# Kernel optimization log

Measured on AMD Instinct MI355X. Metric: run time of the kernel, lower is better.

The kernel has to match this reference:

```python
import jax, jax.numpy as jnp
import numpy as np

EPS = 1e-06


def setup_inputs() -> dict:
    key = jax.random.key(0)
    k1, k2 = jax.random.split(key)
    x = jax.random.normal(k1, (256, 4096), dtype=jnp.float32)
    # learned parameter, init matches torch.randn(...) * 0.1
    shapelets = jax.random.normal(k2, (8, 16, 128), dtype=jnp.float32) * 0.1
    return {"x": x, "shapelets": shapelets}


def reference(x, shapelets):
    B, T = x.shape
    C, Kc, L = shapelets.shape
    nwin = T - L + 1  # stride-1 unfold

    # sliding windows: [B, nwin, L] (same materialization as torch unfold)
    idx = jnp.arange(nwin)[:, None] + jnp.arange(L)[None, :]
    x_win = x[:, idx]

    # z-normalize each window (population std, unbiased=False)
    mu_x = jnp.mean(x_win, axis=2, keepdims=True)
    var_x = jnp.mean((x_win - mu_x) ** 2, axis=2, keepdims=True)
    std_x = jnp.sqrt(var_x) + EPS
    x_norm = (x_win - mu_x) / std_x

    # z-normalize shapelets per class/shapelet
    mu_s = jnp.mean(shapelets, axis=2, keepdims=True)
    var_s = jnp.mean((shapelets - mu_s) ** 2, axis=2, keepdims=True)
    std_s = jnp.sqrt(var_s) + EPS
    s_norm = (shapelets - mu_s) / std_s

    # normalized cross-correlation: [B, nwin, C, Kc]
    corr = jnp.einsum('btl,ckl->btck', x_norm, s_norm) / L

    # max over window positions, concat classes -> [B, C*Kc]
    max_vals = jnp.max(corr, axis=1)  # [B, C, Kc]
    return max_vals.reshape(B, C * Kc)
```

## Files before the change

kernel.cpp:

```cpp
#include <hip/hip_runtime.h>
#include <hip/hip_bf16.h>

typedef __attribute__((ext_vector_type(8))) short short8;
typedef __attribute__((ext_vector_type(4))) float float4v;

#define T_LEN 4096
#define L_LEN 128
#define NWIN  3969
#define CK    128

__device__ __forceinline__ unsigned short f2bf(float f) {
    unsigned u = __float_as_uint(f);
    u += 0x7fffu + ((u >> 16) & 1u);
    return (unsigned short)(u >> 16);
}

__global__ void prep_sh(const float* __restrict__ sh,
                        unsigned short* __restrict__ wsB) {
    const int ck = blockIdx.x;
    const int l  = threadIdx.x;
    __shared__ float rs[2], rq[2];
    const int lane = l & 63, wv = l >> 6;

    float v = sh[ck * L_LEN + l];
    float s = v, q = v * v;
    #pragma unroll
    for (int off = 32; off >= 1; off >>= 1) {
        s += __shfl_xor(s, off);
        q += __shfl_xor(q, off);
    }
    if (lane == 0) { rs[wv] = s; rq[wv] = q; }
    __syncthreads();
    float sm = rs[0] + rs[1], sq = rq[0] + rq[1];
    float mu  = sm * (1.f / L_LEN);
    float var = fmaxf(sq * (1.f / L_LEN) - mu * mu, 0.f);
    float inv = 1.f / (sqrtf(var) + 1e-6f);
    unsigned short b = f2bf((v - mu) * inv);
    const int nt = ck >> 4, n = ck & 15;
    const int kt = l >> 5, qd = (l >> 3) & 3, jj = l & 7;
    wsB[((((nt * 4 + kt) * 64) + qd * 16 + n) << 3) + jj] = b;
}

__global__ __launch_bounds__(512, 2)
void conv_row(const float* __restrict__ x,
              const unsigned short* __restrict__ wsB,
              float* __restrict__ out) {
    __shared__ alignas(16) unsigned short xb[8][T_LEN];
    __shared__ float sty[T_LEN];
    __shared__ float PSs[513], PQs[513];
    __shared__ float grpS[8], grpQ[8];
    __shared__ float wmax[8][CK];

    const int tid  = threadIdx.x;
    const int lane = tid & 63;
    const int wv   = tid >> 6;
    const int row  = blockIdx.x;
    const float4* xr4 = (const float4*)(x + row * T_LEN);

    short8 Bf[8][4];
    {
        const short8* Bp = (const short8*)wsB;
        #pragma unroll
        for (int nt = 0; nt < 8; ++nt)
            #pragma unroll
            for (int kt = 0; kt < 4; ++kt)
                Bf[nt][kt] = Bp[(nt * 4 + kt) * 64 + lane];
    }

    float v[16];
    {
        float4 a0 = xr4[2 * tid];
        float4 a1 = xr4[2 * tid + 1];
        float4 a2 = make_float4(0.f, 0.f, 0.f, 0.f), a3 = a2;
        if (tid < 511) { a2 = xr4[2 * tid + 2]; a3 = xr4[2 * tid + 3]; }
        v[0]=a0.x; v[1]=a0.y; v[2]=a0.z;  v[3]=a0.w;
        v[4]=a1.x; v[5]=a1.y; v[6]=a1.z;  v[7]=a1.w;
        v[8]=a2.x; v[9]=a2.y; v[10]=a2.z; v[11]=a2.w;
        v[12]=a3.x; v[13]=a3.y; v[14]=a3.z; v[15]=a3.w;
    }
    unsigned short bb[16];
    #pragma unroll
    for (int i = 0; i < 16; ++i) bb[i] = f2bf(v[i]);
    #pragma unroll
    for (int c = 0; c < 8; ++c) {
        short8 w8;
        #pragma unroll
        for (int j = 0; j < 8; ++j) w8[j] = (short)bb[c + j];
        *(short8*)&xb[c][8 * tid] = w8;
    }

    float s = 0.f, q = 0.f;
    #pragma unroll
    for (int i = 0; i < 8; ++i) { s += v[i]; q += v[i] * v[i]; }
    float is = s, iq = q;
    #pragma unroll
    for (int off = 1; off < 64; off <<= 1) {
        float ts = __shfl_up(is, off);
        float tq = __shfl_up(iq, off);
        if (lane >= off) { is += ts; iq += tq; }
    }
    if (lane == 63) { grpS[wv] = is; grpQ[wv] = iq; }
    __syncthreads();
    float os = 0.f, oq = 0.f;
    #pragma unroll
    for (int w = 0; w < 7; ++w) if (w < wv) { os += grpS[w]; oq += grpQ[w]; }
    PSs[tid] = os + is - s;
    PQs[tid] = oq + iq - q;
    if (tid == 511) { PSs[512] = os + is; PQs[512] = oq + iq; }
    __syncthreads();

    if (tid < 497) {
        float S = PSs[tid + 16] - PSs[tid];
        float Q = PQs[tid + 16] - PQs[tid];
        float4 b0 = make_float4(0.f, 0.f, 0.f, 0.f), b1 = b0;
        if (tid <= 495) { b0 = xr4[2 * tid + 32]; b1 = xr4[2 * tid + 33]; }
        float xn[8] = {b0.x, b0.y, b0.z, b0.w, b1.x, b1.y, b1.z, b1.w};
        #pragma unroll
        for (int e = 0; e < 8; ++e) {
            int w = 8 * tid + e;
            if (w < NWIN) {
                float mu  = S * (1.f / L_LEN);
                float var = fmaxf(Q * (1.f / L_LEN) - mu * mu, 0.f);
                float sd  = sqrtf(var) + 1e-6f;
                sty[w] = 1.f / (sd * (float)L_LEN);
                S += xn[e] - v[e];
                Q += xn[e] * xn[e] - v[e] * v[e];
            }
        }
    }
    __syncthreads();

    const int abase = (lane & 15) + (lane >> 4);
    const int q4    = (lane >> 4) * 4;
    float vmax[8];
    #pragma unroll
    for (int nt = 0; nt < 8; ++nt) vmax[nt] = -1e30f;

    #pragma unroll 1
    for (int ci = 0; ci < 32; ++ci) {
        const int T0 = (ci < 31) ? ci * 128 : (NWIN - 128);
        const int e0 = T0 + wv;
        const int c  = e0 & 7;
        const int b8 = e0 >> 3;

        float4v acc[8];
        #pragma unroll
        for (int nt = 0; nt < 8; ++nt) acc[nt] = float4v{0.f, 0.f, 0.f, 0.f};

        #pragma unroll
        for (int kt = 0; kt < 4; ++kt) {
            const short8 af = *(const short8*)&xb[c][8 * (b8 + abase + 4 * kt)];
            #pragma unroll
            for (int nt = 0; nt < 8; ++nt)
                acc[nt] = __builtin_amdgcn_mfma_f32_16x16x32_bf16(
                    af, Bf[nt][kt], acc[nt], 0, 0, 0);
        }

        #pragma unroll
        for (int r = 0; r < 4; ++r) {
            const float sr = sty[e0 + 8 * (q4 + r)];
            #pragma unroll
            for (int nt = 0; nt < 8; ++nt)
                vmax[nt] = fmaxf(vmax[nt], acc[nt][r] * sr);
        }
    }

    #pragma unroll
    for (int nt = 0; nt < 8; ++nt) {
        float vx = vmax[nt];
        vx = fmaxf(vx, __shfl_xor(vx, 16));
        vx = fmaxf(vx, __shfl_xor(vx, 32));
        if (lane < 16) wmax[wv][nt * 16 + lane] = vx;
    }
    __syncthreads();
    if (tid < CK) {
        float m = wmax[0][tid];
        #pragma unroll
        for (int w = 1; w < 8; ++w) m = fmaxf(m, wmax[w][tid]);
        out[row * CK + tid] = m;
    }
}

extern "C" void kernel_launch(void* const* d_in, const int* in_sizes, int n_in,
                              void* d_out, int out_size, void* d_ws, size_t ws_size,
                              hipStream_t stream) {
    (void)in_sizes; (void)n_in; (void)out_size; (void)ws_size;
    const float* x  = (const float*)d_in[0];
    const float* sh = (const float*)d_in[1];
    unsigned short* wsB = (unsigned short*)d_ws;
    float* out = (float*)d_out;

    prep_sh<<<128, 128, 0, stream>>>(sh, wsB);
    conv_row<<<256, 512, 0, stream>>>(x, wsB, out);
}
```

Before: 83.02 us.

## Switch correlation GEMM to 32x32x16 MFMA with split-N warp tiling

Replaces the 16x16x32 bf16 MFMA tiling, where each warp covered all 128 shapelets for 16 windows, with 32x32x16 MFMAs. Warps now split into 4 window tiles by 2 shapelet halves, and each warp accumulates two 32x32 tiles over 8 k-steps. The shapelet workspace becomes plain row-major, and the per-phase bf16 x buffers are padded to a 4100 stride, presumably to avoid LDS bank conflicts, which forces 8-byte LDS loads instead of 16-byte ones. The intent is fewer MFMA issues and less register pressure for the B fragments, at the cost of longer dependent MFMA chains per accumulator and more LDS load instructions.

```diff
diff --git a/kernel.cpp b/kernel.cpp
--- a/kernel.cpp
+++ b/kernel.cpp
@@ -1,13 +1,15 @@
 #include <hip/hip_runtime.h>
 #include <hip/hip_bf16.h>
 
-typedef __attribute__((ext_vector_type(8))) short short8;
-typedef __attribute__((ext_vector_type(4))) float float4v;
+typedef __attribute__((ext_vector_type(4)))  short short4v;
+typedef __attribute__((ext_vector_type(8)))  short short8;
+typedef __attribute__((ext_vector_type(16))) float float16v;
 
 #define T_LEN 4096
 #define L_LEN 128
 #define NWIN  3969
 #define CK    128
+#define XSTR  4100
 
 __device__ __forceinline__ unsigned short f2bf(float f) {
     unsigned u = __float_as_uint(f);
@@ -35,21 +37,18 @@
     float mu  = sm * (1.f / L_LEN);
     float var = fmaxf(sq * (1.f / L_LEN) - mu * mu, 0.f);
     float inv = 1.f / (sqrtf(var) + 1e-6f);
-    unsigned short b = f2bf((v - mu) * inv);
-    const int nt = ck >> 4, n = ck & 15;
-    const int kt = l >> 5, qd = (l >> 3) & 3, jj = l & 7;
-    wsB[((((nt * 4 + kt) * 64) + qd * 16 + n) << 3) + jj] = b;
+    wsB[ck * L_LEN + l] = f2bf((v - mu) * inv);
 }
 
 __global__ __launch_bounds__(512, 2)
 void conv_row(const float* __restrict__ x,
               const unsigned short* __restrict__ wsB,
               float* __restrict__ out) {
-    __shared__ alignas(16) unsigned short xb[8][T_LEN];
+    __shared__ alignas(16) unsigned short xb[8 * XSTR];
     __shared__ float sty[T_LEN];
     __shared__ float PSs[513], PQs[513];
     __shared__ float grpS[8], grpQ[8];
-    __shared__ float wmax[8][CK];
+    __shared__ float wmax[8][2][32];
 
     const int tid  = threadIdx.x;
     const int lane = tid & 63;
@@ -57,14 +56,16 @@
     const int row  = blockIdx.x;
     const float4* xr4 = (const float4*)(x + row * T_LEN);
 
-    short8 Bf[8][4];
-    {
-        const short8* Bp = (const short8*)wsB;
-        #pragma unroll
-        for (int nt = 0; nt < 8; ++nt)
-            #pragma unroll
-            for (int kt = 0; kt < 4; ++kt)
-                Bf[nt][kt] = Bp[(nt * 4 + kt) * 64 + lane];
+    const int mt = wv & 3, nh = wv >> 2;
+    const int m32 = lane & 31, h = lane >> 5;
+
+    short8 Bf[2][8];
+    #pragma unroll
+    for (int nt2 = 0; nt2 < 2; ++nt2) {
+        const int ck = 32 * (2 * nh + nt2) + m32;
+        #pragma unroll
+        for (int ks = 0; ks < 8; ++ks)
+            Bf[nt2][ks] = *(const short8*)&wsB[ck * L_LEN + 16 * ks + 8 * h];
     }
 
     float v[16];
@@ -83,10 +84,11 @@
     for (int i = 0; i < 16; ++i) bb[i] = f2bf(v[i]);
     #pragma unroll
     for (int c = 0; c < 8; ++c) {
-        short8 w8;
-        #pragma unroll
-        for (int j = 0; j < 8; ++j) w8[j] = (short)bb[c + j];
-        *(short8*)&xb[c][8 * tid] = w8;
+        short4v lo, hi;
+        #pragma unroll
+        for (int j = 0; j < 4; ++j) { lo[j] = (short)bb[c + j]; hi[j] = (short)bb[c + 4 + j]; }
+        *(short4v*)&xb[c * XSTR + 8 * tid]     = lo;
+        *(short4v*)&xb[c * XSTR + 8 * tid + 4] = hi;
     }
 
     float s = 0.f, q = 0.f;
@@ -130,53 +132,60 @@
     }
     __syncthreads();
 
-    const int abase = (lane & 15) + (lane >> 4);
-    const int q4    = (lane >> 4) * 4;
-    float vmax[8];
-    #pragma unroll
-    for (int nt = 0; nt < 8; ++nt) vmax[nt] = -1e30f;
+    float16v z16;
+    #pragma unroll
+    for (int i = 0; i < 16; ++i) z16[i] = 0.f;
+    float vm0 = -1e30f, vm1 = -1e30f;
 
     #pragma unroll 1
     for (int ci = 0; ci < 32; ++ci) {
         const int T0 = (ci < 31) ? ci * 128 : (NWIN - 128);
-        const int e0 = T0 + wv;
-        const int c  = e0 & 7;
-        const int b8 = e0 >> 3;
-
-        float4v acc[8];
-        #pragma unroll
-        for (int nt = 0; nt < 8; ++nt) acc[nt] = float4v{0.f, 0.f, 0.f, 0.f};
-
-        #pragma unroll
-        for (int kt = 0; kt < 4; ++kt) {
-            const short8 af = *(const short8*)&xb[c][8 * (b8 + abase + 4 * kt)];
+        const int e  = T0 + 32 * mt + m32;
+        const int c  = e & 7;
+        const int rb = e & ~7;
+        const int base = c * XSTR + rb + 8 * h;
+
+        short8 af[8];
+        #pragma unroll
+        for (int ks = 0; ks < 8; ++ks) {
+            short4v lo = *(const short4v*)&xb[base + 16 * ks];
+            short4v hi = *(const short4v*)&xb[base + 16 * ks + 4];
+            af[ks] = __builtin_shufflevector(lo, hi, 0, 1, 2, 3, 4, 5, 6, 7);
+        }
+
+        float sv[16];
+        const int wb = T0 + 32 * mt + 4 * h;
+        #pragma unroll
+        for (int Q = 0; Q < 4; ++Q)
             #pragma unroll
-            for (int nt = 0; nt < 8; ++nt)
-                acc[nt] = __builtin_amdgcn_mfma_f32_16x16x32_bf16(
-                    af, Bf[nt][kt], acc[nt], 0, 0, 0);
-        }
-
-        #pragma unroll
-        for (int r = 0; r < 4; ++r) {
-            const float sr = sty[e0 + 8 * (q4 + r)];
-            #pragma unroll
-            for (int nt = 0; nt < 8; ++nt)
-                vmax[nt] = fmaxf(vmax[nt], acc[nt][r] * sr);
-        }
-    }
-
-    #pragma unroll
-    for (int nt = 0; nt < 8; ++nt) {
-        float vx = vmax[nt];
-        vx = fmaxf(vx, __shfl_xor(vx, 16));
-        vx = fmaxf(vx, __shfl_xor(vx, 32));
-        if (lane < 16) wmax[wv][nt * 16 + lane] = vx;
-    }
+            for (int rr = 0; rr < 4; ++rr)
+                sv[4 * Q + rr] = sty[wb + 8 * Q + rr];
+
+        float16v acc0 = __builtin_amdgcn_mfma_f32_32x32x16_bf16(af[0], Bf[0][0], z16, 0, 0, 0);
+        float16v acc1 = __builtin_amdgcn_mfma_f32_32x32x16_bf16(af[0], Bf[1][0], z16, 0, 0, 0);
+        #pragma unroll
+        for (int ks = 1; ks < 8; ++ks) {
+            acc0 = __builtin_amdgcn_mfma_f32_32x32x16_bf16(af[ks], Bf[0][ks], acc0, 0, 0, 0);
+            acc1 = __builtin_amdgcn_mfma_f32_32x32x16_bf16(af[ks], Bf[1][ks], acc1, 0, 0, 0);
+        }
+
+        #pragma unroll
+        for (int r = 0; r < 16; ++r) {
+            vm0 = fmaxf(vm0, acc0[r] * sv[r]);
+            vm1 = fmaxf(vm1, acc1[r] * sv[r]);
+        }
+    }
+
+    vm0 = fmaxf(vm0, __shfl_xor(vm0, 32));
+    vm1 = fmaxf(vm1, __shfl_xor(vm1, 32));
+    if (lane < 32) { wmax[wv][0][lane] = vm0; wmax[wv][1][lane] = vm1; }
     __syncthreads();
     if (tid < CK) {
-        float m = wmax[0][tid];
-        #pragma unroll
-        for (int w = 1; w < 8; ++w) m = fmaxf(m, wmax[w][tid]);
+        const int dh = tid >> 6, nt2 = (tid >> 5) & 1, c32 = tid & 31;
+        float m = wmax[4 * dh][nt2][c32];
+        #pragma unroll
+        for (int mm = 1; mm < 4; ++mm)
+            m = fmaxf(m, wmax[4 * dh + mm][nt2][c32]);
         out[row * CK + tid] = m;
     }
 }
```

Measured after the change: 89.07 us. 7.3% more time.
